# Kernel optimization log

Hardware: AMD Instinct MI355X
Metric: run time of the kernel (lower is better)

## Reference

```python
import jax, jax.numpy as jnp
import numpy as np

DIM = 2048
N_HEADS = 32
N_KV_HEADS = 4
HEAD_DIM = DIM // N_HEADS  # 64


def _rope_tables(T, head_dim, dtype):
    inv_freq = 1.0 / (10000.0 ** (jnp.arange(0, head_dim, 2, dtype=jnp.float32) / head_dim))
    t = jnp.arange(T, dtype=jnp.float32)
    freqs = jnp.einsum('i,j->ij', t, inv_freq)           # [T, head_dim/2]
    emb = jnp.concatenate([freqs, freqs], axis=-1)        # [T, head_dim]
    return jnp.cos(emb).astype(dtype), jnp.sin(emb).astype(dtype)


def _rotate_half(x):
    d = x.shape[-1] // 2
    return jnp.concatenate([-x[..., d:], x[..., :d]], axis=-1)


def setup_inputs() -> dict:
    key = jax.random.key(0)
    kx, kq, kk, kv, ko = jax.random.split(key, 5)
    s = 1.0 / np.sqrt(DIM)
    return {
        'x': jax.random.normal(kx, (2, 2048, DIM), dtype=jnp.float32),
        'wq': jax.random.normal(kq, (DIM, DIM), dtype=jnp.float32) * s,
        'wk': jax.random.normal(kk, (DIM, DIM // 8), dtype=jnp.float32) * s,
        'wv': jax.random.normal(kv, (DIM, DIM // 8), dtype=jnp.float32) * s,
        'wo': jax.random.normal(ko, (DIM, DIM), dtype=jnp.float32) * s,
    }


def reference(x, wq, wk, wv, wo):
    B, T, C = x.shape
    q = (x @ wq).reshape(B, T, N_HEADS, HEAD_DIM).transpose(0, 2, 1, 3)      # [B,H,T,D]
    k = (x @ wk).reshape(B, T, N_KV_HEADS, HEAD_DIM).transpose(0, 2, 1, 3)   # [B,Hkv,T,D]
    v = (x @ wv).reshape(B, T, N_KV_HEADS, HEAD_DIM).transpose(0, 2, 1, 3)

    cos, sin = _rope_tables(T, HEAD_DIM, x.dtype)  # [T,D]
    q = q * cos + _rotate_half(q) * sin
    k = k * cos + _rotate_half(k) * sin

    rep = N_HEADS // N_KV_HEADS
    k = jnp.repeat(k, rep, axis=1)  # [B,H,T,D]
    v = jnp.repeat(v, rep, axis=1)

    scale = 1.0 / np.sqrt(HEAD_DIM)
    scores = jnp.einsum('bhqd,bhkd->bhqk', q, k) * scale
    causal = jnp.tril(jnp.ones((T, T), dtype=bool))
    scores = jnp.where(causal, scores, jnp.finfo(scores.dtype).min)
    attn = jax.nn.softmax(scores, axis=-1)
    out = jnp.einsum('bhqk,bhkd->bhqd', attn, v)
    out = out.transpose(0, 2, 1, 3).reshape(B, T, C)
    return out @ wo
```

## Files before the change

### kernel.cpp

```cpp
#include <hip/hip_runtime.h>
#include <hip/hip_bf16.h>
#include <stdint.h>

#define DIM 2048
#define TSEQ 2048
#define BATCH 2
#define NH 32
#define NKV 4
#define HD 64
#define MROWS (BATCH*TSEQ)
#define NQKV 2560

typedef __attribute__((ext_vector_type(4))) float f32x4;
typedef __attribute__((ext_vector_type(8))) __bf16 bf16x8;
typedef unsigned short ushort_t;

#define GLDS16(g, l) __builtin_amdgcn_global_load_lds( \
    (const __attribute__((address_space(1))) void*)(g), \
    (__attribute__((address_space(3))) void*)(l), 16, 0, 0)

__device__ __forceinline__ float bflo2f(unsigned int w) {
  union { unsigned int i; float f; } c; c.i = w << 16; return c.f;
}
__device__ __forceinline__ unsigned short f2bf(float f) {
  union { float f; unsigned int i; } c; c.f = f;
  unsigned int x = c.i;
  x += 0x7fffu + ((x >> 16) & 1u);
  return (unsigned short)(x >> 16);
}
__device__ __forceinline__ unsigned short f2bf_fast(float f) {
  union { float f; unsigned int i; } c; c.f = f;
  return (unsigned short)((c.i + 0x8000u) >> 16);
}

__global__ void cast_bf16_k(const float* __restrict__ in, ushort_t* __restrict__ out, int n4) {
  const int i = blockIdx.x * 256 + threadIdx.x;
  if (i >= n4) return;
  const float4 v = ((const float4*)in)[i];
  uint2 p;
  p.x = (unsigned int)f2bf(v.x) | ((unsigned int)f2bf(v.y) << 16);
  p.y = (unsigned int)f2bf(v.z) | ((unsigned int)f2bf(v.w) << 16);
  ((uint2*)out)[i] = p;
}

__global__ void transpose_cast_all(const float* __restrict__ wq, const float* __restrict__ wk,
                                   const float* __restrict__ wv, const float* __restrict__ wo,
                                   ushort_t* __restrict__ wtq, ushort_t* __restrict__ woT) {
  __shared__ float tile[32][33];
  const int by = blockIdx.y;
  const float* src; ushort_t* dst; int N, bnb;
  if (by < 64)      { src = wq; dst = wtq;                    N = DIM; bnb = by; }
  else if (by < 72) { src = wk; dst = wtq + (long)DIM  * DIM; N = 256; bnb = by - 64; }
  else if (by < 80) { src = wv; dst = wtq + (long)2304 * DIM; N = 256; bnb = by - 72; }
  else              { src = wo; dst = woT;                    N = DIM; bnb = by - 80; }
  const int bk = blockIdx.x * 32;
  const int bn = bnb * 32;
  const int tx = threadIdx.x & 31;
  const int ty = threadIdx.x >> 5;
#pragma unroll
  for (int p = 0; p < 4; p++) {
    const int r = ty + p * 8;
    tile[r][tx] = src[(long)(bk + r) * N + bn + tx];
  }
  __syncthreads();
#pragma unroll
  for (int p = 0; p < 4; p++) {
    const int r = ty + p * 8;
    dst[(long)(bn + r) * DIM + bk + tx] = f2bf(tile[tx][r]);
  }
}

#define LOG1E4_D32 0.2878231366242557f
#define QSCALE 0.1803368801111243f

__global__ void rope_tab_k(float2* __restrict__ tab) {
  const int i = blockIdx.x * 256 + threadIdx.x;
  const int t = i >> 5, d = i & 31;
  const float ang = (float)t * __expf(-(float)d * LOG1E4_D32);
  float s_, c_;
  __sincosf(ang, &s_, &c_);
  tab[i] = make_float2(c_, s_);
}

template<int EPI>
__global__ __launch_bounds__(256, 2) void gemm_bt(
    const ushort_t* __restrict__ A, const ushort_t* __restrict__ BT,
    int M, int N, int K,
    float* __restrict__ Cf, ushort_t* __restrict__ Cq,
    ushort_t* __restrict__ Ck, ushort_t* __restrict__ Cv,
    const float2* __restrict__ tab)
{
  __shared__ __align__(16) ushort_t As[128][64];
  __shared__ __align__(16) ushort_t Bs[128][64];
  const int tid  = threadIdx.x;
  const int lane = tid & 63;
  const int wid  = tid >> 6;
  const int wm   = wid >> 1, wn = wid & 1;
  const int l8   = lane >> 3;
  const int c8   = (lane & 7) * 8;
  const long abase = (long)blockIdx.x * 128 * K;
  const long bbase = (long)blockIdx.y * 128 * K;
  const int rsel = lane & 15;
  const int koff = (lane >> 4) * 8;
  f32x4 acc[4][4] = {};

  for (int k0 = 0; k0 < K; k0 += 64) {
    __syncthreads();
#pragma unroll
    for (int i = 0; i < 4; i++) {
      const int r0 = wid * 32 + i * 8;
      GLDS16(&A [abase + (long)(r0 + l8) * K + k0 + c8], &As[r0][0]);
      GLDS16(&BT[bbase + (long)(r0 + l8) * K + k0 + c8], &Bs[r0][0]);
    }
    __syncthreads();
#pragma unroll
    for (int kk = 0; kk < 64; kk += 32) {
      bf16x8 af[4], bfr[4];
#pragma unroll
      for (int m = 0; m < 4; m++) af[m]  = *(const bf16x8*)(&As[wm*64 + m*16 + rsel][kk + koff]);
#pragma unroll
      for (int n = 0; n < 4; n++) bfr[n] = *(const bf16x8*)(&Bs[wn*64 + n*16 + rsel][kk + koff]);
#pragma unroll
      for (int m = 0; m < 4; m++)
#pragma unroll
        for (int n = 0; n < 4; n++)
          acc[m][n] = __builtin_amdgcn_mfma_f32_16x16x32_bf16(af[m], bfr[n], acc[m][n], 0, 0, 0);
    }
  }

  const int rbase = blockIdx.x * 128 + wm * 64 + (lane >> 4) * 4;
  const int l15e  = lane & 15;

  if (EPI == 1) {
    const int cbase = blockIdx.y * 128 + wn * 64 + l15e;
#pragma unroll
    for (int m = 0; m < 4; m++)
#pragma unroll
      for (int n = 0; n < 4; n++) {
        const int gn = cbase + n * 16;
#pragma unroll
        for (int j = 0; j < 4; j++)
          Cf[(long)(rbase + m * 16 + j) * N + gn] = acc[m][n][j];
      }
  } else {
    const int colbase = blockIdx.y * 128 + wn * 64;
    if (colbase >= DIM + 256) {
#pragma unroll
      for (int m = 0; m < 4; m++) {
        const int gm0 = rbase + m * 16;
        const int b = gm0 >> 11;
        const int t = gm0 & (TSEQ - 1);
#pragma unroll
        for (int n = 0; n < 4; n++) {
          const int x = colbase + n * 16 + l15e - DIM;
          const int hkv = (x >> 6) & 3;
          const int d = x & 63;
          uint2 pk;
          pk.x = (unsigned int)f2bf(acc[m][n][0]) | ((unsigned int)f2bf(acc[m][n][1]) << 16);
          pk.y = (unsigned int)f2bf(acc[m][n][2]) | ((unsigned int)f2bf(acc[m][n][3]) << 16);
          *(uint2*)(&Cv[((long)(b * NKV + hkv) * HD + d) * TSEQ + t]) = pk;
        }
      }
    } else {
      const bool isQ = (colbase < DIM);
      const int hkv = (colbase - DIM) >> 6;
#pragma unroll
      for (int m = 0; m < 4; m++) {
#pragma unroll
        for (int j = 0; j < 4; j++) {
          const int gm = rbase + m * 16 + j;
          const int t = gm & (TSEQ - 1);
          const int b = gm >> 11;
          const float2 cs0 = tab[t * 32 + l15e];
          const float2 cs1 = tab[t * 32 + 16 + l15e];
          const float v0 = acc[m][0][j], v1 = acc[m][1][j];
          const float v2 = acc[m][2][j], v3 = acc[m][3][j];
          const float r0 = v0 * cs0.x - v2 * cs0.y;
          const float r2 = v2 * cs0.x + v0 * cs0.y;
          const float r1 = v1 * cs1.x - v3 * cs1.y;
          const float r3 = v3 * cs1.x + v1 * cs1.y;
          if (isQ) {
            const long base = (long)gm * DIM + colbase + l15e;
            Cq[base]      = f2bf(r0 * QSCALE);
            Cq[base + 16] = f2bf(r1 * QSCALE);
            Cq[base + 32] = f2bf(r2 * QSCALE);
            Cq[base + 48] = f2bf(r3 * QSCALE);
          } else {
            const long base = ((long)(b * NKV + hkv) * TSEQ + t) * HD + l15e;
            Ck[base]      = f2bf(r0);
            Ck[base + 16] = f2bf(r1);
            Ck[base + 32] = f2bf(r2);
            Ck[base + 48] = f2bf(r3);
          }
        }
      }
    }
  }
}

__global__ __launch_bounds__(512, 4) void attn_mfma(
    const ushort_t* __restrict__ q, const ushort_t* __restrict__ k,
    const ushort_t* __restrict__ vt, ushort_t* __restrict__ o)
{
  __shared__ __align__(16) ushort_t Ks[2][64][64];
  __shared__ __align__(16) ushort_t Vs[2][64][64];

  const int tid  = threadIdx.x;
  const int lane = tid & 63;
  const int wid  = tid >> 6;
  const int l15  = lane & 15;
  const int lg   = lane >> 4;
  const int od   = lg & 1;
  const int hi   = lg >> 1;
  const int sw   = l15 & 7;

  const int bh  = blockIdx.x & 63;
  const int qt  = (TSEQ / 256 - 1) - (blockIdx.x >> 6);
  const int h   = bh & (NH - 1);
  const int b   = bh >> 5;
  const int hkv = h >> 3;
  const int qbase = qt * 256;
  const int qw0   = qbase + wid * 32;

  bf16x8 qf[2][2];
#pragma unroll
  for (int hh = 0; hh < 2; hh++) {
    const ushort_t* qp = q + ((long)(b * TSEQ) + qw0 + hh * 16 + l15) * DIM + h * 64 + lg * 8;
    qf[hh][0] = *(const bf16x8*)(qp);
    qf[hh][1] = *(const bf16x8*)(qp + 32);
  }

  const ushort_t* kb_ = k  + (long)(b * NKV + hkv) * TSEQ * HD;
  const ushort_t* vb_ = vt + (long)(b * NKV + hkv) * HD * TSEQ;

  float l_c[2] = {0.f, 0.f};
  f32x4 o_[2][4] = {};

  const int srow = tid >> 3;
  const int sgc  = (tid & 7) * 8;
  const int slc  = (((tid & 7) ^ (srow & 7))) * 8;

  const int gv0 = ((0 + 2 * od + hi) ^ sw) * 8;
  const int gv1 = ((4 + 2 * od + hi) ^ sw) * 8;

  const int nkv = 4 * (qt + 1);

  *(uint4*)(&Ks[0][srow][slc]) = *(const uint4*)(&kb_[(long)srow * HD + sgc]);
  *(uint4*)(&Vs[0][srow][slc]) = *(const uint4*)(&vb_[(long)srow * TSEQ + sgc]);
  int cur = 0;

  for (int kbv = 0; kbv < nkv; kbv++) {
    const int kb0 = kbv * 64;
    const bool pf = (kbv + 1 < nkv);
    uint4 kr = {}, vr = {};
    if (pf) {
      kr = *(const uint4*)(&kb_[(long)(kb0 + 64 + srow) * HD + sgc]);
      vr = *(const uint4*)(&vb_[(long)srow * TSEQ + kb0 + 64 + sgc]);
    }
    asm volatile("s_waitcnt lgkmcnt(0)\n\ts_barrier" ::: "memory");

#pragma unroll
    for (int hh = 0; hh < 2; hh++) {
      const int qh0 = qw0 + hh * 16;
      if (kb0 <= qh0 + 15) {
        f32x4 st[4] = {};
#pragma unroll
        for (int kt = 0; kt < 4; kt++) {
#pragma unroll
          for (int c = 0; c < 2; c++) {
            const bf16x8 kf = *(const bf16x8*)(&Ks[cur][kt * 16 + l15][((4*c + lg) ^ sw) * 8]);
            st[kt] = __builtin_amdgcn_mfma_f32_16x16x32_bf16(kf, qf[hh][c], st[kt], 0, 0, 0);
          }
        }

        if (kb0 + 63 > qh0) {
          const int qg = qh0 + l15;
#pragma unroll
          for (int kt = 0; kt < 4; kt++) {
            const int kg0 = kb0 + kt * 16 + lg * 4;
#pragma unroll
            for (int j = 0; j < 4; j++) {
              if (kg0 + j > qg) st[kt][j] = -1e30f;
            }
          }
        }

        unsigned int u00, u01, u10, u11, u20, u21, u30, u31;
#define PACK_KT(KT, UA, UB) { \
          const float p0 = exp2f(st[KT][0]); \
          const float p1 = exp2f(st[KT][1]); \
          const float p2 = exp2f(st[KT][2]); \
          const float p3 = exp2f(st[KT][3]); \
          l_c[hh] += (p0 + p1) + (p2 + p3); \
          asm("v_cvt_pk_bf16_f32 %0, %1, %2" : "=v"(UA) : "v"(p0), "v"(p1)); \
          asm("v_cvt_pk_bf16_f32 %0, %1, %2" : "=v"(UB) : "v"(p2), "v"(p3)); \
        }
        PACK_KT(0, u00, u01)
        PACK_KT(1, u10, u11)
        PACK_KT(2, u20, u21)
        PACK_KT(3, u30, u31)
#undef PACK_KT

        const unsigned int r00 = __shfl_xor((int)(od ? u00 : u10), 16, 64);
        const unsigned int r01 = __shfl_xor((int)(od ? u01 : u11), 16, 64);
        const unsigned int r10 = __shfl_xor((int)(od ? u20 : u30), 16, 64);
        const unsigned int r11 = __shfl_xor((int)(od ? u21 : u31), 16, 64);
        union { unsigned int u[4]; bf16x8 v; } T0, T1;
        T0.u[0] = od ? r00 : u00;  T0.u[1] = od ? r01 : u01;
        T0.u[2] = od ? u10 : r00;  T0.u[3] = od ? u11 : r01;
        T1.u[0] = od ? r10 : u20;  T1.u[1] = od ? r11 : u21;
        T1.u[2] = od ? u30 : r10;  T1.u[3] = od ? u31 : r11;

#pragma unroll
        for (int nt = 0; nt < 4; nt++) {
          const bf16x8 vf0 = *(const bf16x8*)(&Vs[cur][nt * 16 + l15][gv0]);
          o_[hh][nt] = __builtin_amdgcn_mfma_f32_16x16x32_bf16(T0.v, vf0, o_[hh][nt], 0, 0, 0);
        }
#pragma unroll
        for (int nt = 0; nt < 4; nt++) {
          const bf16x8 vf1 = *(const bf16x8*)(&Vs[cur][nt * 16 + l15][gv1]);
          o_[hh][nt] = __builtin_amdgcn_mfma_f32_16x16x32_bf16(T1.v, vf1, o_[hh][nt], 0, 0, 0);
        }
      }
    }

    if (pf) {
      *(uint4*)(&Ks[cur ^ 1][srow][slc]) = kr;
      *(uint4*)(&Vs[cur ^ 1][srow][slc]) = vr;
    }
    cur ^= 1;
  }

#pragma unroll
  for (int hh = 0; hh < 2; hh++) {
    float lc = l_c[hh];
    lc += __shfl_xor(lc, 16, 64);
    lc += __shfl_xor(lc, 32, 64);
    const long orow = (long)(b * TSEQ) + qw0 + hh * 16;
#pragma unroll
    for (int j = 0; j < 4; j++) {
      const float inv = 1.f / __shfl(lc, (lane & 48) | (lg * 4 + j), 64);
#pragma unroll
      for (int nt = 0; nt < 4; nt++)
        o[(orow + lg * 4 + j) * DIM + h * 64 + nt * 16 + l15] = f2bf_fast(o_[hh][nt][j] * inv);
    }
  }
}

extern "C" void kernel_launch(void* const* d_in, const int* in_sizes, int n_in,
                              void* d_out, int out_size, void* d_ws, size_t ws_size,
                              hipStream_t stream) {
  const float* x  = (const float*)d_in[0];
  const float* wq = (const float*)d_in[1];
  const float* wk = (const float*)d_in[2];
  const float* wv = (const float*)d_in[3];
  const float* wo = (const float*)d_in[4];
  float* out = (float*)d_out;

  ushort_t* ws = (ushort_t*)d_ws;
  const long NXB = (long)MROWS * DIM;
  ushort_t* xb   = ws;
  ushort_t* wtq  = xb  + NXB;
  ushort_t* woT  = wtq + (long)NQKV * DIM;
  ushort_t* qws  = woT + (long)DIM * DIM;
  ushort_t* kws  = qws + NXB;
  ushort_t* vtws = kws + (long)BATCH * NKV * TSEQ * HD;
  ushort_t* aws  = vtws + (long)BATCH * NKV * TSEQ * HD;
  float2*   tab  = (float2*)(aws + NXB);

  cast_bf16_k<<<(int)(NXB / 1024), 256, 0, stream>>>(x, xb, (int)(NXB / 4));
  transpose_cast_all<<<dim3(64, 144), 256, 0, stream>>>(wq, wk, wv, wo, wtq, woT);
  rope_tab_k<<<256, 256, 0, stream>>>(tab);

  gemm_bt<0><<<dim3(32, 20), 256, 0, stream>>>(xb, wtq, MROWS, NQKV, DIM,
                                               nullptr, qws, kws, vtws, tab);

  attn_mfma<<<BATCH * NH * (TSEQ / 256), 512, 0, stream>>>(qws, kws, vtws, aws);

  gemm_bt<1><<<dim3(32, 16), 256, 0, stream>>>(aws, woT, MROWS, DIM, DIM,
                                               out, nullptr, nullptr, nullptr, nullptr);
}
```

Before: 210.9 us.

## Pair causal query tiles per block to balance attention work

Each attention block now processes two 128-row query tiles, one early and one late (pq and 15-pq), sharing the K/V stream loaded for the longer tile. Previously blocks owned one 256-row tile, so causal masking gave some blocks eight times more kv iterations than others. Pairing evens out per-block work and reduces tail imbalance. The cost is that the short tile's skip checks still run on every iteration, and register state for two accumulators persists.

```diff
diff --git a/kernel.cpp b/kernel.cpp
--- a/kernel.cpp
+++ b/kernel.cpp
@@ -215,26 +215,30 @@
   const int sw   = l15 & 7;
 
   const int bh  = blockIdx.x & 63;
-  const int qt  = (TSEQ / 256 - 1) - (blockIdx.x >> 6);
+  const int pq  = blockIdx.x >> 6;
+  const int qtA = 15 - pq;
+  const int qtB = pq;
   const int h   = bh & (NH - 1);
   const int b   = bh >> 5;
   const int hkv = h >> 3;
-  const int qbase = qt * 256;
-  const int qw0   = qbase + wid * 32;
-
-  bf16x8 qf[2][2];
-#pragma unroll
-  for (int hh = 0; hh < 2; hh++) {
-    const ushort_t* qp = q + ((long)(b * TSEQ) + qw0 + hh * 16 + l15) * DIM + h * 64 + lg * 8;
-    qf[hh][0] = *(const bf16x8*)(qp);
-    qf[hh][1] = *(const bf16x8*)(qp + 32);
+  const int qA0 = qtA * 128 + wid * 16;
+  const int qB0 = qtB * 128 + wid * 16;
+
+  bf16x8 qfA0, qfA1, qfB0, qfB1;
+  {
+    const ushort_t* qp = q + ((long)(b * TSEQ) + qA0 + l15) * DIM + h * 64 + lg * 8;
+    qfA0 = *(const bf16x8*)(qp);
+    qfA1 = *(const bf16x8*)(qp + 32);
+    const ushort_t* qp2 = q + ((long)(b * TSEQ) + qB0 + l15) * DIM + h * 64 + lg * 8;
+    qfB0 = *(const bf16x8*)(qp2);
+    qfB1 = *(const bf16x8*)(qp2 + 32);
   }
 
   const ushort_t* kb_ = k  + (long)(b * NKV + hkv) * TSEQ * HD;
   const ushort_t* vb_ = vt + (long)(b * NKV + hkv) * HD * TSEQ;
 
-  float l_c[2] = {0.f, 0.f};
-  f32x4 o_[2][4] = {};
+  float lA = 0.f, lB = 0.f;
+  f32x4 oA[4] = {}, oB[4] = {};
 
   const int srow = tid >> 3;
   const int sgc  = (tid & 7) * 8;
@@ -243,11 +247,68 @@
   const int gv0 = ((0 + 2 * od + hi) ^ sw) * 8;
   const int gv1 = ((4 + 2 * od + hi) ^ sw) * 8;
 
-  const int nkv = 4 * (qt + 1);
+  const int nkv = 2 * (qtA + 1);
 
   *(uint4*)(&Ks[0][srow][slc]) = *(const uint4*)(&kb_[(long)srow * HD + sgc]);
   *(uint4*)(&Vs[0][srow][slc]) = *(const uint4*)(&vb_[(long)srow * TSEQ + sgc]);
   int cur = 0;
+
+#define PROC_TILE(QF0, QF1, OO, LL, Q0) \
+  if (kb0 <= (Q0) + 15) { \
+    f32x4 st[4] = {}; \
+    _Pragma("unroll") \
+    for (int kt = 0; kt < 4; kt++) { \
+      const bf16x8 kf0 = *(const bf16x8*)(&Ks[cur][kt * 16 + l15][((0 + lg) ^ sw) * 8]); \
+      st[kt] = __builtin_amdgcn_mfma_f32_16x16x32_bf16(kf0, QF0, st[kt], 0, 0, 0); \
+      const bf16x8 kf1 = *(const bf16x8*)(&Ks[cur][kt * 16 + l15][((4 + lg) ^ sw) * 8]); \
+      st[kt] = __builtin_amdgcn_mfma_f32_16x16x32_bf16(kf1, QF1, st[kt], 0, 0, 0); \
+    } \
+    if (kb0 + 63 > (Q0)) { \
+      const int qg = (Q0) + l15; \
+      _Pragma("unroll") \
+      for (int kt = 0; kt < 4; kt++) { \
+        const int kg0 = kb0 + kt * 16 + lg * 4; \
+        _Pragma("unroll") \
+        for (int j = 0; j < 4; j++) { \
+          if (kg0 + j > qg) st[kt][j] = -1e30f; \
+        } \
+      } \
+    } \
+    unsigned int u00, u01, u10, u11, u20, u21, u30, u31; \
+    PACK_KT(0, u00, u01, LL) \
+    PACK_KT(1, u10, u11, LL) \
+    PACK_KT(2, u20, u21, LL) \
+    PACK_KT(3, u30, u31, LL) \
+    const unsigned int r00 = __shfl_xor((int)(od ? u00 : u10), 16, 64); \
+    const unsigned int r01 = __shfl_xor((int)(od ? u01 : u11), 16, 64); \
+    const unsigned int r10 = __shfl_xor((int)(od ? u20 : u30), 16, 64); \
+    const unsigned int r11 = __shfl_xor((int)(od ? u21 : u31), 16, 64); \
+    union { unsigned int u[4]; bf16x8 v; } T0, T1; \
+    T0.u[0] = od ? r00 : u00;  T0.u[1] = od ? r01 : u01; \
+    T0.u[2] = od ? u10 : r00;  T0.u[3] = od ? u11 : r01; \
+    T1.u[0] = od ? r10 : u20;  T1.u[1] = od ? r11 : u21; \
+    T1.u[2] = od ? u30 : r10;  T1.u[3] = od ? u31 : r11; \
+    _Pragma("unroll") \
+    for (int nt = 0; nt < 4; nt++) { \
+      const bf16x8 vf0 = *(const bf16x8*)(&Vs[cur][nt * 16 + l15][gv0]); \
+      OO[nt] = __builtin_amdgcn_mfma_f32_16x16x32_bf16(T0.v, vf0, OO[nt], 0, 0, 0); \
+    } \
+    _Pragma("unroll") \
+    for (int nt = 0; nt < 4; nt++) { \
+      const bf16x8 vf1 = *(const bf16x8*)(&Vs[cur][nt * 16 + l15][gv1]); \
+      OO[nt] = __builtin_amdgcn_mfma_f32_16x16x32_bf16(T1.v, vf1, OO[nt], 0, 0, 0); \
+    } \
+  }
+
+#define PACK_KT(KT, UA, UB, LL) { \
+    const float p0 = exp2f(st[KT][0]); \
+    const float p1 = exp2f(st[KT][1]); \
+    const float p2 = exp2f(st[KT][2]); \
+    const float p3 = exp2f(st[KT][3]); \
+    LL += (p0 + p1) + (p2 + p3); \
+    asm("v_cvt_pk_bf16_f32 %0, %1, %2" : "=v"(UA) : "v"(p0), "v"(p1)); \
+    asm("v_cvt_pk_bf16_f32 %0, %1, %2" : "=v"(UB) : "v"(p2), "v"(p3)); \
+  }
 
   for (int kbv = 0; kbv < nkv; kbv++) {
     const int kb0 = kbv * 64;
@@ -259,70 +320,8 @@
     }
     asm volatile("s_waitcnt lgkmcnt(0)\n\ts_barrier" ::: "memory");
 
-#pragma unroll
-    for (int hh = 0; hh < 2; hh++) {
-      const int qh0 = qw0 + hh * 16;
-      if (kb0 <= qh0 + 15) {
-        f32x4 st[4] = {};
-#pragma unroll
-        for (int kt = 0; kt < 4; kt++) {
-#pragma unroll
-          for (int c = 0; c < 2; c++) {
-            const bf16x8 kf = *(const bf16x8*)(&Ks[cur][kt * 16 + l15][((4*c + lg) ^ sw) * 8]);
-            st[kt] = __builtin_amdgcn_mfma_f32_16x16x32_bf16(kf, qf[hh][c], st[kt], 0, 0, 0);
-          }
-        }
-
-        if (kb0 + 63 > qh0) {
-          const int qg = qh0 + l15;
-#pragma unroll
-          for (int kt = 0; kt < 4; kt++) {
-            const int kg0 = kb0 + kt * 16 + lg * 4;
-#pragma unroll
-            for (int j = 0; j < 4; j++) {
-              if (kg0 + j > qg) st[kt][j] = -1e30f;
-            }
-          }
-        }
-
-        unsigned int u00, u01, u10, u11, u20, u21, u30, u31;
-#define PACK_KT(KT, UA, UB) { \
-          const float p0 = exp2f(st[KT][0]); \
-          const float p1 = exp2f(st[KT][1]); \
-          const float p2 = exp2f(st[KT][2]); \
-          const float p3 = exp2f(st[KT][3]); \
-          l_c[hh] += (p0 + p1) + (p2 + p3); \
-          asm("v_cvt_pk_bf16_f32 %0, %1, %2" : "=v"(UA) : "v"(p0), "v"(p1)); \
-          asm("v_cvt_pk_bf16_f32 %0, %1, %2" : "=v"(UB) : "v"(p2), "v"(p3)); \
-        }
-        PACK_KT(0, u00, u01)
-        PACK_KT(1, u10, u11)
-        PACK_KT(2, u20, u21)
-        PACK_KT(3, u30, u31)
-#undef PACK_KT
-
-        const unsigned int r00 = __shfl_xor((int)(od ? u00 : u10), 16, 64);
-        const unsigned int r01 = __shfl_xor((int)(od ? u01 : u11), 16, 64);
-        const unsigned int r10 = __shfl_xor((int)(od ? u20 : u30), 16, 64);
-        const unsigned int r11 = __shfl_xor((int)(od ? u21 : u31), 16, 64);
-        union { unsigned int u[4]; bf16x8 v; } T0, T1;
-        T0.u[0] = od ? r00 : u00;  T0.u[1] = od ? r01 : u01;
-        T0.u[2] = od ? u10 : r00;  T0.u[3] = od ? u11 : r01;
-        T1.u[0] = od ? r10 : u20;  T1.u[1] = od ? r11 : u21;
-        T1.u[2] = od ? u30 : r10;  T1.u[3] = od ? u31 : r11;
-
-#pragma unroll
-        for (int nt = 0; nt < 4; nt++) {
-          const bf16x8 vf0 = *(const bf16x8*)(&Vs[cur][nt * 16 + l15][gv0]);
-          o_[hh][nt] = __builtin_amdgcn_mfma_f32_16x16x32_bf16(T0.v, vf0, o_[hh][nt], 0, 0, 0);
-        }
-#pragma unroll
-        for (int nt = 0; nt < 4; nt++) {
-          const bf16x8 vf1 = *(const bf16x8*)(&Vs[cur][nt * 16 + l15][gv1]);
-          o_[hh][nt] = __builtin_amdgcn_mfma_f32_16x16x32_bf16(T1.v, vf1, o_[hh][nt], 0, 0, 0);
-        }
-      }
-    }
+    PROC_TILE(qfA0, qfA1, oA, lA, qA0)
+    PROC_TILE(qfB0, qfB1, oB, lB, qB0)
 
     if (pf) {
       *(uint4*)(&Ks[cur ^ 1][srow][slc]) = kr;
@@ -330,19 +329,33 @@
     }
     cur ^= 1;
   }
-
-#pragma unroll
-  for (int hh = 0; hh < 2; hh++) {
-    float lc = l_c[hh];
+#undef PROC_TILE
+#undef PACK_KT
+
+  {
+    float lc = lA;
     lc += __shfl_xor(lc, 16, 64);
     lc += __shfl_xor(lc, 32, 64);
-    const long orow = (long)(b * TSEQ) + qw0 + hh * 16;
+    const long orow = (long)(b * TSEQ) + qA0;
 #pragma unroll
     for (int j = 0; j < 4; j++) {
       const float inv = 1.f / __shfl(lc, (lane & 48) | (lg * 4 + j), 64);
 #pragma unroll
       for (int nt = 0; nt < 4; nt++)
-        o[(orow + lg * 4 + j) * DIM + h * 64 + nt * 16 + l15] = f2bf_fast(o_[hh][nt][j] * inv);
+        o[(orow + lg * 4 + j) * DIM + h * 64 + nt * 16 + l15] = f2bf_fast(oA[nt][j] * inv);
+    }
+  }
+  {
+    float lc = lB;
+    lc += __shfl_xor(lc, 16, 64);
+    lc += __shfl_xor(lc, 32, 64);
+    const long orow = (long)(b * TSEQ) + qB0;
+#pragma unroll
+    for (int j = 0; j < 4; j++) {
+      const float inv = 1.f / __shfl(lc, (lane & 48) | (lg * 4 + j), 64);
+#pragma unroll
+      for (int nt = 0; nt < 4; nt++)
+        o[(orow + lg * 4 + j) * DIM + h * 64 + nt * 16 + l15] = f2bf_fast(oB[nt][j] * inv);
     }
   }
 }
@@ -375,7 +388,7 @@
   gemm_bt<0><<<dim3(32, 20), 256, 0, stream>>>(xb, wtq, MROWS, NQKV, DIM,
                                                nullptr, qws, kws, vtws, tab);
 
-  attn_mfma<<<BATCH * NH * (TSEQ / 256), 512, 0, stream>>>(qws, kws, vtws, aws);
+  attn_mfma<<<BATCH * NH * 8, 512, 0, stream>>>(qws, kws, vtws, aws);
 
   gemm_bt<1><<<dim3(32, 16), 256, 0, stream>>>(aws, woT, MROWS, DIM, DIM,
                                                out, nullptr, nullptr, nullptr, nullptr);
```

Measured after the change: 200.2 us. 5.1% less time.
